# Kernel optimization log

Measured on AMD Instinct MI355X. Metric: run time of the kernel, lower is better.

## Reference

```python
import jax, jax.numpy as jnp
from jax import lax
import numpy as np

B, N, NF, EF, MD = 16, 128, 9, 3, 5
H, D, FF, L, O = 24, 768, 3072, 12, 128
NA, NID, NOD, NE, NS, NED = 4608, 256, 256, 1536, 512, 128
S = N + 1
EPS = 1e-5


def setup_inputs() -> dict:
    key = jax.random.key(0)
    ks = iter(jax.random.split(key, 64))
    emb_s = 0.02
    lin_s = 0.02 / np.sqrt(L)

    def nrm(shape, s):
        return jax.random.normal(next(ks), shape, jnp.float32) * s

    inp = {
        'x': jax.random.randint(next(ks), (B, N, NF), 0, NA + 1),
        'in_degree': jax.random.randint(next(ks), (B, N), 0, NID),
        'out_degree': jax.random.randint(next(ks), (B, N), 0, NOD),
        'spatial_pos': jax.random.randint(next(ks), (B, N, N), 0, NS),
        'edge_input': jax.random.randint(next(ks), (B, N, N, MD, EF), 0, NE + 1),
        'attn_bias': jnp.zeros((B, S, S), jnp.float32),
        # embeddings (padding_idx=0 rows zeroed)
        'atom_emb': nrm((NA + 1, D), emb_s).at[0].set(0.0),
        'in_deg_emb': nrm((NID, D), emb_s).at[0].set(0.0),
        'out_deg_emb': nrm((NOD, D), emb_s).at[0].set(0.0),
        'graph_token': nrm((1, D), emb_s),
        'edge_emb': nrm((NE + 1, H), emb_s).at[0].set(0.0),
        'edge_dis_emb': nrm((NED, H, H), emb_s),
        'spatial_emb': nrm((NS, H), emb_s).at[0].set(0.0),
        'virt_dist': nrm((1, H), emb_s),
        # stacked per-layer params
        'ln1_g': jnp.ones((L, D)), 'ln1_b': jnp.zeros((L, D)),
        'wq': nrm((L, D, D), lin_s), 'bq': jnp.zeros((L, D)),
        'wk': nrm((L, D, D), lin_s), 'bk': jnp.zeros((L, D)),
        'wv': nrm((L, D, D), lin_s), 'bv': jnp.zeros((L, D)),
        'wo': nrm((L, D, D), lin_s), 'bo': jnp.zeros((L, D)),
        'ln2_g': jnp.ones((L, D)), 'ln2_b': jnp.zeros((L, D)),
        'w1': nrm((L, D, FF), lin_s), 'b1': jnp.zeros((L, FF)),
        'w2': nrm((L, FF, D), lin_s), 'b2': jnp.zeros((L, D)),
        'final_g': jnp.ones((D,)), 'final_b': jnp.zeros((D,)),
        'out_w': nrm((D, O), lin_s), 'out_b': jnp.zeros((O,)),
    }
    return inp


def _ln(v, g, b):
    m = v.mean(-1, keepdims=True)
    va = ((v - m) ** 2).mean(-1, keepdims=True)
    return (v - m) / jnp.sqrt(va + EPS) * g + b


def _forward(x, in_degree, out_degree, spatial_pos, edge_input, attn_bias,
             atom_emb, in_deg_emb, out_deg_emb, graph_token,
             edge_emb, edge_dis_emb, spatial_emb, virt_dist,
             ln1_g, ln1_b, wq, bq, wk, bk, wv, bv, wo, bo,
             ln2_g, ln2_b, w1, b1, w2, b2, final_g, final_b, out_w, out_b):
    nb = x.shape[0]
    # ---- graph attn bias ----
    # spatial bias [B,H,N,N]
    sp_bias = spatial_emb[spatial_pos].transpose(0, 3, 1, 2)
    # multi-hop edge bias
    sp_ = jnp.where(spatial_pos == 0, 1, spatial_pos)
    sp_ = jnp.where(sp_ > 1, sp_ - 1, sp_)
    sp_ = jnp.clip(sp_, 0, MD)
    ei = edge_emb[edge_input].mean(-2)                       # [B,N,N,MD,H]
    eo = jnp.einsum('bijdh,dhk->bijk', ei, edge_dis_emb[:MD])
    edge_bias = (eo / sp_[..., None].astype(jnp.float32)).transpose(0, 3, 1, 2)
    t = virt_dist.reshape(1, H, 1)                           # virtual-token distance
    gab = jnp.repeat(attn_bias[:, None], H, axis=1)          # [B,H,S,S]
    gab = gab.at[:, :, 1:, 1:].add(sp_bias + edge_bias)
    gab = gab.at[:, :, 1:, 0].add(t)
    gab = gab.at[:, :, 0, :].add(t)
    gab = gab + attn_bias[:, None]
    # ---- node features ----
    nf = atom_emb[x].sum(-2) + in_deg_emb[in_degree] + out_deg_emb[out_degree]
    h = jnp.concatenate([jnp.broadcast_to(graph_token[None], (nb, 1, D)), nf], axis=1)  # [B,S,D]
    dk = D // H
    scale = dk ** -0.5

    def step(hc, p):
        (g1, b1n, Wq, Bq, Wk, Bk, Wv, Bv, Wo, Bo, g2, b2n, W1, B1, W2, B2) = p
        y = _ln(hc, g1, b1n)
        q = (y @ Wq + Bq).reshape(nb, S, H, dk).transpose(0, 2, 1, 3) * scale
        k = (y @ Wk + Bk).reshape(nb, S, H, dk).transpose(0, 2, 1, 3)
        v = (y @ Wv + Bv).reshape(nb, S, H, dk).transpose(0, 2, 1, 3)
        att = jnp.einsum('bhqd,bhkd->bhqk', q, k) + gab
        att = jax.nn.softmax(att, axis=-1)
        ctx = jnp.einsum('bhqk,bhkd->bhqd', att, v)
        ctx = ctx.transpose(0, 2, 1, 3).reshape(nb, S, D)
        hc = hc + (ctx @ Wo + Bo)
        y = _ln(hc, g2, b2n)
        y = jax.nn.gelu(y @ W1 + B1, approximate=False) @ W2 + B2
        return hc + y, None

    h, _ = lax.scan(step, h, (ln1_g, ln1_b, wq, bq, wk, bk, wv, bv, wo, bo,
                              ln2_g, ln2_b, w1, b1, w2, b2))
    h = _ln(h, final_g, final_b)
    return h[:, 0] @ out_w + out_b  # [B,O]


def reference(x, in_degree, out_degree, spatial_pos, edge_input, attn_bias,
              atom_emb, in_deg_emb, out_deg_emb, graph_token,
              edge_emb, edge_dis_emb, spatial_emb, virt_dist,
              ln1_g, ln1_b, wq, bq, wk, bk, wv, bv, wo, bo,
              ln2_g, ln2_b, w1, b1, w2, b2, final_g, final_b, out_w, out_b):
    return _forward(x, in_degree, out_degree, spatial_pos, edge_input, attn_bias,
                    atom_emb, in_deg_emb, out_deg_emb, graph_token,
                    edge_emb, edge_dis_emb, spatial_emb, virt_dist,
                    ln1_g, ln1_b, wq, bq, wk, bk, wv, bv, wo, bo,
                    ln2_g, ln2_b, w1, b1, w2, b2, final_g, final_b, out_w, out_b)
```

## Files before the change

kernel.cpp:

```cpp
#include <hip/hip_runtime.h>
#include <hip/hip_bf16.h>
#include <math.h>

typedef __hip_bfloat16 bf16;
typedef __attribute__((ext_vector_type(8))) short short8;
typedef __attribute__((ext_vector_type(4))) short short4v;
typedef __attribute__((ext_vector_type(4))) float f32x4;

constexpr int NB = 16;
constexpr int ND = 128;
constexpr int SQ = 129;
constexpr int NH = 24;
constexpr int DM = 768;
constexpr int DF = 3072;
constexpr int NLAY = 12;
constexpr int MROWS = NB * SQ;

__device__ __forceinline__ short f2bs(float f) {
  bf16 h = __float2bfloat16(f);
  return *(short*)&h;
}

__device__ __forceinline__ void gload16(const void* g, void* lds) {
  __builtin_amdgcn_global_load_lds(
      (const __attribute__((address_space(1))) unsigned int*)g,
      (__attribute__((address_space(3))) unsigned int*)lds, 16, 0, 0);
}

__global__ void k_nodefeat(const int* __restrict__ x, const int* __restrict__ ind,
                           const int* __restrict__ outd,
                           const float* __restrict__ atom, const float* __restrict__ ide,
                           const float* __restrict__ ode, const float* __restrict__ gtok,
                           float* __restrict__ h) {
  int bs = blockIdx.x;
  int b = bs / SQ, s = bs % SQ;
  int t = threadIdx.x;
  float* hrow = h + (size_t)bs * DM;
  if (s == 0) {
    for (int c = t; c < DM; c += 256) hrow[c] = gtok[c];
  } else {
    int n = s - 1;
    const int* xr = x + (b * ND + n) * 9;
    int a0 = xr[0], a1 = xr[1], a2 = xr[2], a3 = xr[3], a4 = xr[4];
    int a5 = xr[5], a6 = xr[6], a7 = xr[7], a8 = xr[8];
    int ii = ind[b * ND + n], oo = outd[b * ND + n];
    for (int c = t; c < DM; c += 256) {
      float acc = ide[(size_t)ii * DM + c] + ode[(size_t)oo * DM + c];
      acc += atom[(size_t)a0 * DM + c];
      acc += atom[(size_t)a1 * DM + c];
      acc += atom[(size_t)a2 * DM + c];
      acc += atom[(size_t)a3 * DM + c];
      acc += atom[(size_t)a4 * DM + c];
      acc += atom[(size_t)a5 * DM + c];
      acc += atom[(size_t)a6 * DM + c];
      acc += atom[(size_t)a7 * DM + c];
      acc += atom[(size_t)a8 * DM + c];
      hrow[c] = acc;
    }
  }
}

__global__ void k_gab_border(const float* __restrict__ ab, const float* __restrict__ virt,
                             float* __restrict__ gab) {
  int b = blockIdx.x;
  const int tot = NH * SQ + NH * ND;
  for (int idx = threadIdx.x; idx < tot; idx += 256) {
    if (idx < NH * SQ) {
      int hh = idx / SQ, j = idx % SQ;
      float v = 2.f * ab[((size_t)b * SQ + 0) * SQ + j] + virt[hh];
      gab[(((size_t)b * NH + hh) * SQ + 0) * SQ + j] = v;
    } else {
      int r = idx - NH * SQ;
      int hh = r / ND, i = r % ND + 1;
      float v = 2.f * ab[((size_t)b * SQ + i) * SQ + 0] + virt[hh];
      gab[(((size_t)b * NH + hh) * SQ + i) * SQ + 0] = v;
    }
  }
}

__global__ __launch_bounds__(256) void k_gab_edge(
    const int* __restrict__ spos, const int* __restrict__ eidx,
    const float* __restrict__ eemb, const float* __restrict__ edemb,
    const float* __restrict__ semb, const float* __restrict__ ab,
    float* __restrict__ gab) {
  __shared__ int eidxs[960];
  __shared__ short ei2[64 * 136];
  __shared__ short edT[32 * 136];
  __shared__ float ot[24][65];
  __shared__ float rinvA[64], a2A[64];
  __shared__ int spA[64];
  int bi = blockIdx.x;
  int half = bi & 1;
  int i = (bi >> 1) & 127;
  int b = bi >> 8;
  int j0 = half * 64;
  int t = threadIdx.x;
  const size_t rowbase = ((size_t)(b * ND + i)) * ND + j0;

  const int* esrc = eidx + rowbase * 15;
  for (int idx = t; idx < 960; idx += 256) eidxs[idx] = esrc[idx];
  for (int u = t; u < 720; u += 256) {
    int dh = u / 6, kq = u % 6;
    f32x4 v = *(const f32x4*)&edemb[dh * 24 + kq * 4];
    edT[(kq * 4 + 0) * 136 + dh] = f2bs(v[0]);
    edT[(kq * 4 + 1) * 136 + dh] = f2bs(v[1]);
    edT[(kq * 4 + 2) * 136 + dh] = f2bs(v[2]);
    edT[(kq * 4 + 3) * 136 + dh] = f2bs(v[3]);
  }
  for (int u = t; u < 1472; u += 256) {
    int k, dh;
    if (u < 384) { k = u >> 4; dh = 120 + (u & 15); }
    else { int v = u - 384; k = 24 + v / 136; dh = v % 136; }
    edT[k * 136 + dh] = 0;
  }
  if (t < 64) {
    int j = t;
    int sp = spos[rowbase + j];
    int spc = (sp == 0) ? 1 : sp;
    spc = (spc > 1) ? spc - 1 : spc;
    if (spc > 5) spc = 5;
    spA[j] = sp;
    rinvA[j] = 1.f / (float)spc;
    a2A[j] = 2.f * ab[((size_t)b * SQ + (i + 1)) * SQ + (j0 + j + 1)];
  }
  __syncthreads();

  {
    int j = t & 63, d = t >> 6;
#pragma unroll
    for (int pass = 0; pass < 2; pass++) {
      if (pass == 1) {
        if (t >= 64) break;
        j = t; d = 4;
      }
      const int* ep = &eidxs[j * 15 + d * 3];
      const float* r0 = eemb + (size_t)ep[0] * NH;
      const float* r1 = eemb + (size_t)ep[1] * NH;
      const float* r2 = eemb + (size_t)ep[2] * NH;
#pragma unroll
      for (int hq = 0; hq < 6; hq++) {
        f32x4 s = (*(const f32x4*)&r0[hq * 4] + *(const f32x4*)&r1[hq * 4] +
                   *(const f32x4*)&r2[hq * 4]) * (1.f / 3.f);
        short4v o;
        o[0] = f2bs(s[0]); o[1] = f2bs(s[1]); o[2] = f2bs(s[2]); o[3] = f2bs(s[3]);
        *(short4v*)&ei2[j * 136 + d * 24 + hq * 4] = o;
      }
    }
  }
  for (int idx = t; idx < 64 * 8; idx += 256) {
    int j = idx >> 3;
    ei2[j * 136 + 120 + (idx & 7)] = 0;
  }
  __syncthreads();

  int lane = t & 63, w = t >> 6;
  int fr = lane & 15, q = lane >> 4, fo = q * 8;
  f32x4 acc0 = {0.f, 0.f, 0.f, 0.f}, acc1 = {0.f, 0.f, 0.f, 0.f};
#pragma unroll
  for (int kk = 0; kk < 4; kk++) {
    short8 af = *(const short8*)&ei2[(w * 16 + fr) * 136 + kk * 32 + fo];
    short8 b0 = *(const short8*)&edT[(fr) * 136 + kk * 32 + fo];
    short8 b1 = *(const short8*)&edT[(16 + fr) * 136 + kk * 32 + fo];
    acc0 = __builtin_amdgcn_mfma_f32_16x16x32_bf16(af, b0, acc0, 0, 0, 0);
    acc1 = __builtin_amdgcn_mfma_f32_16x16x32_bf16(af, b1, acc1, 0, 0, 0);
  }
#pragma unroll
  for (int e = 0; e < 4; e++) {
    int j = w * 16 + q * 4 + e;
    ot[fr][j] = acc0[e];
    if (fr < 8) ot[16 + fr][j] = acc1[e];
  }
  __syncthreads();
  size_t obase = (((size_t)b * NH) * SQ + (i + 1)) * SQ + (j0 + 1);
  for (int idx = t; idx < 24 * 64; idx += 256) {
    int k = idx >> 6, j = idx & 63;
    float v = a2A[j] + semb[spA[j] * NH + k] + ot[k][j] * rinvA[j];
    gab[obase + (size_t)k * SQ * SQ + j] = v;
  }
}

struct Ptrs4 { const float* p[4]; };

template <int NW>
__global__ void k_transpose(Ptrs4 ps, short* __restrict__ dst, int R, int C,
                            size_t sstride) {
  __shared__ short tile[64][68];
  int z = blockIdx.z;
  const float* src = ps.p[z % NW] + (size_t)(z / NW) * sstride;
  short* d = dst + (size_t)z * (size_t)R * C;
  int r0 = blockIdx.x * 64, c0 = blockIdx.y * 64;
  int t = threadIdx.x;
  int tr = t >> 4, tc = (t & 15) * 4;
#pragma unroll
  for (int i = 0; i < 4; i++) {
    int r = tr + i * 16;
    f32x4 v = *(const f32x4*)(src + (size_t)(r0 + r) * C + c0 + tc);
    tile[r][tc + 0] = f2bs(v[0]);
    tile[r][tc + 1] = f2bs(v[1]);
    tile[r][tc + 2] = f2bs(v[2]);
    tile[r][tc + 3] = f2bs(v[3]);
  }
  __syncthreads();
#pragma unroll
  for (int i = 0; i < 4; i++) {
    int rr = tr + i * 16;
    short4v o;
    o[0] = tile[tc + 0][rr];
    o[1] = tile[tc + 1][rr];
    o[2] = tile[tc + 2][rr];
    o[3] = tile[tc + 3][rr];
    *(short4v*)(d + (size_t)(c0 + rr) * R + r0 + tc) = o;
  }
}

__global__ void k_ln(const float* __restrict__ h, const float* __restrict__ g,
                     const float* __restrict__ bb, bf16* __restrict__ y) {
  int r = blockIdx.x;
  int t = threadIdx.x, lane = t & 63, wid = t >> 6;
  __shared__ float red[8];
  const float* row = h + (size_t)r * DM;
  float v0 = row[t], v1 = row[t + 256], v2 = row[t + 512];
  float s = v0 + v1 + v2;
#pragma unroll
  for (int o = 32; o > 0; o >>= 1) s += __shfl_xor(s, o);
  if (lane == 0) red[wid] = s;
  __syncthreads();
  float mean = (red[0] + red[1] + red[2] + red[3]) * (1.f / 768.f);
  float d0 = v0 - mean, d1 = v1 - mean, d2 = v2 - mean;
  float q = d0 * d0 + d1 * d1 + d2 * d2;
#pragma unroll
  for (int o = 32; o > 0; o >>= 1) q += __shfl_xor(q, o);
  if (lane == 0) red[4 + wid] = q;
  __syncthreads();
  float var = (red[4] + red[5] + red[6] + red[7]) * (1.f / 768.f);
  float rstd = rsqrtf(var + 1e-5f);
  bf16* yr = y + (size_t)r * DM;
  yr[t] = __float2bfloat16(d0 * rstd * g[t] + bb[t]);
  yr[t + 256] = __float2bfloat16(d1 * rstd * g[t + 256] + bb[t + 256]);
  yr[t + 512] = __float2bfloat16(d2 * rstd * g[t + 512] + bb[t + 512]);
}

__global__ void k_ln_add2(float* __restrict__ h, const float* __restrict__ p0,
                          const float* __restrict__ p1, const float* __restrict__ cb,
                          const float* __restrict__ g, const float* __restrict__ bb,
                          bf16* __restrict__ y) {
  int r = blockIdx.x;
  int t = threadIdx.x, lane = t & 63, wid = t >> 6;
  __shared__ float red[8];
  size_t base = (size_t)r * DM;
  float v0 = h[base + t] + p0[base + t] + p1[base + t] + cb[t];
  float v1 = h[base + t + 256] + p0[base + t + 256] + p1[base + t + 256] + cb[t + 256];
  float v2 = h[base + t + 512] + p0[base + t + 512] + p1[base + t + 512] + cb[t + 512];
  h[base + t] = v0;
  h[base + t + 256] = v1;
  h[base + t + 512] = v2;
  float s = v0 + v1 + v2;
#pragma unroll
  for (int o = 32; o > 0; o >>= 1) s += __shfl_xor(s, o);
  if (lane == 0) red[wid] = s;
  __syncthreads();
  float mean = (red[0] + red[1] + red[2] + red[3]) * (1.f / 768.f);
  float d0 = v0 - mean, d1 = v1 - mean, d2 = v2 - mean;
  float q = d0 * d0 + d1 * d1 + d2 * d2;
#pragma unroll
  for (int o = 32; o > 0; o >>= 1) q += __shfl_xor(q, o);
  if (lane == 0) red[4 + wid] = q;
  __syncthreads();
  float var = (red[4] + red[5] + red[6] + red[7]) * (1.f / 768.f);
  float rstd = rsqrtf(var + 1e-5f);
  bf16* yr = y + base;
  yr[t] = __float2bfloat16(d0 * rstd * g[t] + bb[t]);
  yr[t + 256] = __float2bfloat16(d1 * rstd * g[t + 256] + bb[t + 256]);
  yr[t + 512] = __float2bfloat16(d2 * rstd * g[t + 512] + bb[t + 512]);
}

struct GemmPtrs {
  const short* bt[3];
  const float* bias[3];
  void* out[3];
  int aoff[3];
};

template <int MODE>
__device__ __forceinline__ void gemm_store(void* outp, size_t idx, float v) {
  if (MODE == 0 || MODE == 3) {
    ((float*)outp)[idx] = v;
  } else if (MODE == 4) {
    ((bf16*)outp)[idx] = __float2bfloat16(v);
  } else {
    float gg = 0.5f * v * (1.f + erff(v * 0.70710678118654752f));
    ((bf16*)outp)[idx] = __float2bfloat16(gg);
  }
}

template <int MODE>
__global__ __launch_bounds__(256, 3) void k_gemm128(const short* __restrict__ A, GemmPtrs p,
                                                    int M, int N, int K, int lda, int ldb) {
  __shared__ short At[128 * 64];
  __shared__ short Bt[128 * 64];
  int z = blockIdx.z;
  const short* BT = p.bt[z];
  const float* bias = p.bias[z];
  A += p.aoff[z];
  int m0 = blockIdx.x * 128, n0 = blockIdx.y * 128;
  int t = threadIdx.x, lane = t & 63, wid = t >> 6;
  int wr = wid >> 1, wc = wid & 1;
  f32x4 acc[4][4];
#pragma unroll
  for (int a = 0; a < 4; a++)
#pragma unroll
    for (int c = 0; c < 4; c++) acc[a][c] = (f32x4){0.f, 0.f, 0.f, 0.f};

  int lrow8 = lane >> 3;
  int lseg = (lane & 7) ^ lrow8;
  const short* gA[4];
  const short* gB[4];
#pragma unroll
  for (int i = 0; i < 4; i++) {
    int ar = m0 + wid * 32 + i * 8 + lrow8;
    if (ar >= M) ar = M - 1;
    gA[i] = A + (size_t)ar * lda + lseg * 8;
    int br = n0 + wid * 32 + i * 8 + lrow8;
    gB[i] = BT + (size_t)br * ldb + lseg * 8;
  }

  const int NIT = K >> 6;
  int fr = lane & 15, q = lane >> 4;
  for (int it = 0; it < NIT; ++it) {
    int k0 = it << 6;
#pragma unroll
    for (int i = 0; i < 4; i++) {
      gload16(gA[i] + k0, &At[(wid * 32 + i * 8) * 64]);
      gload16(gB[i] + k0, &Bt[(wid * 32 + i * 8) * 64]);
    }
    __syncthreads();
#pragma unroll
    for (int kk = 0; kk < 2; kk++) {
      int sg = ((q + kk * 4) ^ (fr & 7)) * 8;
      short8 af[4], bf[4];
#pragma unroll
      for (int mr = 0; mr < 4; mr++)
        af[mr] = *(const short8*)&At[(wr * 64 + mr * 16 + fr) * 64 + sg];
#pragma unroll
      for (int nc = 0; nc < 4; nc++)
        bf[nc] = *(const short8*)&Bt[(wc * 64 + nc * 16 + fr) * 64 + sg];
#pragma unroll
      for (int mr = 0; mr < 4; mr++)
#pragma unroll
        for (int nc = 0; nc < 4; nc++)
          acc[mr][nc] = __builtin_amdgcn_mfma_f32_16x16x32_bf16(af[mr], bf[nc], acc[mr][nc], 0, 0, 0);
    }
    __syncthreads();
  }

  int rsub = q * 4;
#pragma unroll
  for (int nc = 0; nc < 4; nc++) {
    int col = n0 + wc * 64 + nc * 16 + fr;
    float bv = (MODE == 3) ? 0.f : bias[col];
#pragma unroll
    for (int mr = 0; mr < 4; mr++) {
#pragma unroll
      for (int e = 0; e < 4; e++) {
        int r = m0 + wr * 64 + mr * 16 + rsub + e;
        if (r < M) gemm_store<MODE>(p.out[z], (size_t)r * N + col, acc[mr][nc][e] + bv);
      }
    }
  }
}

template <int MODE>
__global__ __launch_bounds__(256, 4) void k_gemm64(const short* __restrict__ A, GemmPtrs p,
                                                   int M, int N, int K, int lda, int ldb) {
  __shared__ short At[64 * 64];
  __shared__ short Bt[128 * 64];
  int z = blockIdx.z;
  const short* BT = p.bt[z];
  const float* bias = p.bias[z];
  A += p.aoff[z];
  int m0 = blockIdx.x * 64, n0 = blockIdx.y * 128;
  int t = threadIdx.x, lane = t & 63, wid = t >> 6;
  int wr = wid >> 1, wc = wid & 1;
  f32x4 acc[2][4];
#pragma unroll
  for (int a = 0; a < 2; a++)
#pragma unroll
    for (int c = 0; c < 4; c++) acc[a][c] = (f32x4){0.f, 0.f, 0.f, 0.f};

  int lrow8 = lane >> 3;
  int lseg = (lane & 7) ^ lrow8;
  const short* gA[2];
  const short* gB[4];
#pragma unroll
  for (int i = 0; i < 2; i++) {
    int ar = m0 + wid * 16 + i * 8 + lrow8;
    if (ar >= M) ar = M - 1;
    gA[i] = A + (size_t)ar * lda + lseg * 8;
  }
#pragma unroll
  for (int i = 0; i < 4; i++) {
    int br = n0 + wid * 32 + i * 8 + lrow8;
    gB[i] = BT + (size_t)br * ldb + lseg * 8;
  }

  const int NIT = K >> 6;
  int fr = lane & 15, q = lane >> 4;
  for (int it = 0; it < NIT; ++it) {
    int k0 = it << 6;
#pragma unroll
    for (int i = 0; i < 2; i++) gload16(gA[i] + k0, &At[(wid * 16 + i * 8) * 64]);
#pragma unroll
    for (int i = 0; i < 4; i++) gload16(gB[i] + k0, &Bt[(wid * 32 + i * 8) * 64]);
    __syncthreads();
#pragma unroll
    for (int kk = 0; kk < 2; kk++) {
      int sg = ((q + kk * 4) ^ (fr & 7)) * 8;
      short8 af[2], bf[4];
#pragma unroll
      for (int mr = 0; mr < 2; mr++)
        af[mr] = *(const short8*)&At[(wr * 32 + mr * 16 + fr) * 64 + sg];
#pragma unroll
      for (int nc = 0; nc < 4; nc++)
        bf[nc] = *(const short8*)&Bt[(wc * 64 + nc * 16 + fr) * 64 + sg];
#pragma unroll
      for (int mr = 0; mr < 2; mr++)
#pragma unroll
        for (int nc = 0; nc < 4; nc++)
          acc[mr][nc] = __builtin_amdgcn_mfma_f32_16x16x32_bf16(af[mr], bf[nc], acc[mr][nc], 0, 0, 0);
    }
    __syncthreads();
  }

  int rsub = q * 4;
#pragma unroll
  for (int nc = 0; nc < 4; nc++) {
    int col = n0 + wc * 64 + nc * 16 + fr;
    float bv = (MODE == 3) ? 0.f : bias[col];
#pragma unroll
    for (int mr = 0; mr < 2; mr++) {
#pragma unroll
      for (int e = 0; e < 4; e++) {
        int r = m0 + wr * 32 + mr * 16 + rsub + e;
        if (r < M) gemm_store<MODE>(p.out[z], (size_t)r * N + col, acc[mr][nc][e] + bv);
      }
    }
  }
}

__global__ __launch_bounds__(256) void k_attn(const bf16* __restrict__ Q,
                                              const bf16* __restrict__ Kb,
                                              const bf16* __restrict__ Vb,
                                              const float* __restrict__ gab,
                                              bf16* __restrict__ ctx) {
  __shared__ short Ql[144 * 40];
  __shared__ short Kl[144 * 40];
  __shared__ short Vt[32 * 168];
  __shared__ short Pc[144 * 40];
  int bh = blockIdx.x;
  int b = bh / NH, hh = bh % NH;
  int t = threadIdx.x;
  for (int idx = t; idx < 32 * 40; idx += 256) {
    int d = idx / 40, kk = 128 + (idx % 40);
    Vt[d * 168 + kk] = 0;
  }
  for (int idx = t; idx < 129 * 4; idx += 256) {
    int s = idx >> 2, seg = idx & 3;
    size_t src = ((size_t)(b * SQ + s)) * DM + hh * 32 + seg * 8;
    *(short8*)&Ql[s * 40 + seg * 8] = *(const short8*)((const short*)Q + src);
    *(short8*)&Kl[s * 40 + seg * 8] = *(const short8*)((const short*)Kb + src);
  }
  for (int idx = t; idx < 15 * 4; idx += 256) {
    int s = 129 + (idx >> 2), seg = idx & 3;
    short8 zz = {0, 0, 0, 0, 0, 0, 0, 0};
    *(short8*)&Ql[s * 40 + seg * 8] = zz;
    *(short8*)&Kl[s * 40 + seg * 8] = zz;
  }
  for (int idx = t; idx < 129 * 4; idx += 256) {
    int kk = idx >> 2, seg = idx & 3;
    size_t src = ((size_t)(b * SQ + kk)) * DM + hh * 32 + seg * 8;
    short8 v = *(const short8*)((const short*)Vb + src);
#pragma unroll
    for (int j = 0; j < 8; j++) Vt[(seg * 8 + j) * 168 + kk] = v[j];
  }
  __syncthreads();

  int lane = t & 63, w = t >> 6;
  int c16 = lane & 15, q4 = lane >> 4;
  const float scale = 0.17677669529663689f;
  const float* gabp = gab + (((size_t)(b * NH + hh)) * SQ) * SQ;

  for (int mt = w; mt < 9; mt += 4) {
    f32x4 sc[9];
    short8 aq = *(const short8*)&Ql[(mt * 16 + c16) * 40 + q4 * 8];
#pragma unroll
    for (int nt = 0; nt < 9; nt++) {
      short8 bk = *(const short8*)&Kl[(nt * 16 + c16) * 40 + q4 * 8];
      f32x4 zz = {0.f, 0.f, 0.f, 0.f};
      sc[nt] = __builtin_amdgcn_mfma_f32_16x16x32_bf16(aq, bk, zz, 0, 0, 0);
    }
#pragma unroll
    for (int e = 0; e < 4; e++) {
      int row = mt * 16 + q4 * 4 + e;
      int rr = row < 129 ? row : 128;
      const float* grow = gabp + (size_t)rr * SQ;
      float mloc = -1e30f;
#pragma unroll
      for (int nt = 0; nt < 9; nt++) {
        int col = nt * 16 + c16;
        float s = (col < 129) ? (sc[nt][e] * scale + grow[col]) : -1e30f;
        sc[nt][e] = s;
        mloc = fmaxf(mloc, s);
      }
#pragma unroll
      for (int o = 1; o < 16; o <<= 1) mloc = fmaxf(mloc, __shfl_xor(mloc, o));
      float sum = 0.f;
#pragma unroll
      for (int nt = 0; nt < 9; nt++) {
        float pp = __expf(sc[nt][e] - mloc);
        sc[nt][e] = pp;
        sum += pp;
      }
#pragma unroll
      for (int o = 1; o < 16; o <<= 1) sum += __shfl_xor(sum, o);
      float inv = 1.f / sum;
#pragma unroll
      for (int nt = 0; nt < 9; nt++) sc[nt][e] *= inv;
    }
    f32x4 oacc0 = {0.f, 0.f, 0.f, 0.f}, oacc1 = {0.f, 0.f, 0.f, 0.f};
#pragma unroll
    for (int c = 0; c < 5; c++) {
#pragma unroll
      for (int u = 0; u < 2; u++) {
        int nt = c * 2 + u;
        if (nt < 9) {
#pragma unroll
          for (int e = 0; e < 4; e++)
            Pc[(mt * 16 + q4 * 4 + e) * 40 + u * 16 + c16] = f2bs(sc[nt][e]);
        } else {
#pragma unroll
          for (int e = 0; e < 4; e++)
            Pc[(mt * 16 + q4 * 4 + e) * 40 + u * 16 + c16] = 0;
        }
      }
      asm volatile("s_waitcnt lgkmcnt(0)" ::: "memory");
      __builtin_amdgcn_sched_barrier(0);
      short8 ap = *(const short8*)&Pc[(mt * 16 + c16) * 40 + q4 * 8];
      short8 bv0 = *(const short8*)&Vt[(c16) * 168 + c * 32 + q4 * 8];
      short8 bv1 = *(const short8*)&Vt[(16 + c16) * 168 + c * 32 + q4 * 8];
      oacc0 = __builtin_amdgcn_mfma_f32_16x16x32_bf16(ap, bv0, oacc0, 0, 0, 0);
      oacc1 = __builtin_amdgcn_mfma_f32_16x16x32_bf16(ap, bv1, oacc1, 0, 0, 0);
    }
#pragma unroll
    for (int e = 0; e < 4; e++) {
      int row = mt * 16 + q4 * 4 + e;
      if (row < 129) {
        size_t obase = ((size_t)(b * SQ + row)) * DM + hh * 32;
        ctx[obase + c16] = __float2bfloat16(oacc0[e]);
        ctx[obase + 16 + c16] = __float2bfloat16(oacc1[e]);
      }
    }
  }
}

__global__ void k_final_add2(const float* __restrict__ h, const float* __restrict__ p0,
                             const float* __restrict__ p1, const float* __restrict__ cb,
                             const float* __restrict__ g, const float* __restrict__ bb,
                             const float* __restrict__ ow, const float* __restrict__ ob,
                             float* __restrict__ out) {
  int b = blockIdx.x;
  int t = threadIdx.x, lane = t & 63, wid = t >> 6;
  __shared__ float red[8];
  __shared__ float yn[768];
  size_t base = (size_t)(b * SQ) * DM;
  float v0 = h[base + t] + p0[base + t] + p1[base + t] + cb[t];
  float v1 = h[base + t + 256] + p0[base + t + 256] + p1[base + t + 256] + cb[t + 256];
  float v2 = h[base + t + 512] + p0[base + t + 512] + p1[base + t + 512] + cb[t + 512];
  float s = v0 + v1 + v2;
#pragma unroll
  for (int o = 32; o > 0; o >>= 1) s += __shfl_xor(s, o);
  if (lane == 0) red[wid] = s;
  __syncthreads();
  float mean = (red[0] + red[1] + red[2] + red[3]) * (1.f / 768.f);
  float d0 = v0 - mean, d1 = v1 - mean, d2 = v2 - mean;
  float q = d0 * d0 + d1 * d1 + d2 * d2;
#pragma unroll
  for (int o = 32; o > 0; o >>= 1) q += __shfl_xor(q, o);
  if (lane == 0) red[4 + wid] = q;
  __syncthreads();
  float var = (red[4] + red[5] + red[6] + red[7]) * (1.f / 768.f);
  float rstd = rsqrtf(var + 1e-5f);
  yn[t] = d0 * rstd * g[t] + bb[t];
  yn[t + 256] = d1 * rstd * g[t + 256] + bb[t + 256];
  yn[t + 512] = d2 * rstd * g[t + 512] + bb[t + 512];
  __syncthreads();
  if (t < 128) {
    float acc = ob[t];
    for (int d = 0; d < 768; d++) acc += yn[d] * ow[d * 128 + t];
    out[b * 128 + t] = acc;
  }
}

extern "C" void kernel_launch(void* const* d_in, const int* in_sizes, int n_in,
                              void* d_out, int out_size, void* d_ws, size_t ws_size,
                              hipStream_t stream) {
  (void)in_sizes; (void)n_in; (void)out_size;
  const int* x     = (const int*)d_in[0];
  const int* ind   = (const int*)d_in[1];
  const int* outd  = (const int*)d_in[2];
  const int* spos  = (const int*)d_in[3];
  const int* eidx  = (const int*)d_in[4];
  const float* ab   = (const float*)d_in[5];
  const float* atom = (const float*)d_in[6];
  const float* ide  = (const float*)d_in[7];
  const float* ode  = (const float*)d_in[8];
  const float* gtok = (const float*)d_in[9];
  const float* eemb = (const float*)d_in[10];
  const float* edemb= (const float*)d_in[11];
  const float* semb = (const float*)d_in[12];
  const float* virt = (const float*)d_in[13];
  const float* ln1g = (const float*)d_in[14];
  const float* ln1b = (const float*)d_in[15];
  const float* wq  = (const float*)d_in[16];
  const float* bq   = (const float*)d_in[17];
  const float* wk  = (const float*)d_in[18];
  const float* bk   = (const float*)d_in[19];
  const float* wv  = (const float*)d_in[20];
  const float* bv   = (const float*)d_in[21];
  const float* wo  = (const float*)d_in[22];
  const float* bo   = (const float*)d_in[23];
  const float* ln2g = (const float*)d_in[24];
  const float* ln2b = (const float*)d_in[25];
  const float* w1  = (const float*)d_in[26];
  const float* b1   = (const float*)d_in[27];
  const float* w2  = (const float*)d_in[28];
  const float* b2   = (const float*)d_in[29];
  const float* fg   = (const float*)d_in[30];
  const float* fb   = (const float*)d_in[31];
  const float* ow   = (const float*)d_in[32];
  const float* ob   = (const float*)d_in[33];
  float* out = (float*)d_out;

  const int DD2 = DM * DM;
  const size_t WQKVO = (size_t)DD2;
  const size_t WFF = (size_t)DM * DF;

  char* ws = (char*)d_ws;
  size_t off = 0;
  auto alloc = [&](size_t bytes) -> void* {
    void* p = ws + off;
    off += (bytes + 255) & ~(size_t)255;
    return p;
  };
  float* gab = (float*)alloc((size_t)NB * NH * SQ * SQ * 4);
  float* h   = (float*)alloc((size_t)MROWS * DM * 4);
  bf16* y    = (bf16*)alloc((size_t)MROWS * DM * 2);
  bf16* qb   = (bf16*)alloc((size_t)MROWS * DM * 2);
  bf16* kb2  = (bf16*)alloc((size_t)MROWS * DM * 2);
  bf16* vb2  = (bf16*)alloc((size_t)MROWS * DM * 2);
  bf16* ctx  = (bf16*)alloc((size_t)MROWS * DM * 2);
  bf16* t1   = (bf16*)alloc((size_t)MROWS * DF * 2);
  float* p0  = (float*)alloc((size_t)MROWS * DM * 4);
  float* p1  = (float*)alloc((size_t)MROWS * DM * 4);

  size_t need_hoist = off + ((size_t)NLAY * 4 * WQKVO + 2 * (size_t)NLAY * WFF) * 2 + (1 << 20);
  bool hoist = ws_size >= need_hoist;
  short* wT  = (short*)alloc((hoist ? (size_t)NLAY * 4 * WQKVO : 4 * WQKVO) * 2);
  short* w1T = (short*)alloc((hoist ? (size_t)NLAY * WFF : WFF) * 2);
  short* w2T = (short*)alloc((hoist ? (size_t)NLAY * WFF : WFF) * 2);

  dim3 blk(256);
  k_nodefeat<<<dim3(NB * SQ), blk, 0, stream>>>(x, ind, outd, atom, ide, ode, gtok, h);
  k_gab_border<<<dim3(NB), blk, 0, stream>>>(ab, virt, gab);
  k_gab_edge<<<dim3(NB * ND * 2), blk, 0, stream>>>(spos, eidx, eemb, edemb, semb, ab, gab);

  if (hoist) {
    Ptrs4 pq; pq.p[0] = wq; pq.p[1] = wk; pq.p[2] = wv; pq.p[3] = wo;
    k_transpose<4><<<dim3(12, 12, 48), blk, 0, stream>>>(pq, wT, DM, DM, WQKVO);
    Ptrs4 pa; pa.p[0] = w1; pa.p[1] = pa.p[2] = pa.p[3] = w1;
    k_transpose<1><<<dim3(12, 48, 12), blk, 0, stream>>>(pa, w1T, DM, DF, WFF);
    Ptrs4 pb; pb.p[0] = w2; pb.p[1] = pb.p[2] = pb.p[3] = w2;
    k_transpose<1><<<dim3(48, 12, 12), blk, 0, stream>>>(pb, w2T, DF, DM, WFF);
  }

  for (int l = 0; l < NLAY; l++) {
    if (!hoist) {
      Ptrs4 pq;
      pq.p[0] = wq + (size_t)l * DD2; pq.p[1] = wk + (size_t)l * DD2;
      pq.p[2] = wv + (size_t)l * DD2; pq.p[3] = wo + (size_t)l * DD2;
      k_transpose<4><<<dim3(12, 12, 4), blk, 0, stream>>>(pq, wT, DM, DM, 0);
      Ptrs4 pa; pa.p[0] = w1 + (size_t)l * WFF; pa.p[1] = pa.p[2] = pa.p[3] = pa.p[0];
      k_transpose<1><<<dim3(12, 48, 1), blk, 0, stream>>>(pa, w1T, DM, DF, 0);
      Ptrs4 pb; pb.p[0] = w2 + (size_t)l * WFF; pb.p[1] = pb.p[2] = pb.p[3] = pb.p[0];
      k_transpose<1><<<dim3(48, 12, 1), blk, 0, stream>>>(pb, w2T, DF, DM, 0);
    }
    const short* wTl  = wT  + (hoist ? (size_t)l * 4 * WQKVO : 0);
    const short* w1Tl = w1T + (hoist ? (size_t)l * WFF : 0);
    const short* w2Tl = w2T + (hoist ? (size_t)l * WFF : 0);

    if (l == 0)
      k_ln<<<dim3(MROWS), blk, 0, stream>>>(h, ln1g, ln1b, y);

    GemmPtrs gq;
    gq.bt[0] = wTl; gq.bt[1] = wTl + DD2; gq.bt[2] = wTl + 2 * DD2;
    gq.bias[0] = bq + l * DM; gq.bias[1] = bk + l * DM; gq.bias[2] = bv + l * DM;
    gq.out[0] = qb; gq.out[1] = kb2; gq.out[2] = vb2;
    gq.aoff[0] = gq.aoff[1] = gq.aoff[2] = 0;
    k_gemm128<4><<<dim3(17, 6, 3), blk, 0, stream>>>((const short*)y, gq, MROWS, DM, DM, DM, DM);

    k_attn<<<dim3(NB * NH), blk, 0, stream>>>(qb, kb2, vb2, gab, ctx);

    GemmPtrs go;
    go.bt[0] = wTl + 3 * DD2; go.bt[1] = wTl + 3 * DD2 + 384;
    go.bias[0] = go.bias[1] = nullptr;
    go.out[0] = p0; go.out[1] = p1;
    go.aoff[0] = 0; go.aoff[1] = 384;
    go.bt[2] = go.bt[0]; go.out[2] = p0; go.aoff[2] = 0; go.bias[2] = nullptr;
    k_gemm64<3><<<dim3(33, 6, 2), blk, 0, stream>>>((const short*)ctx, go, MROWS, DM, 384, DM, DM);

    k_ln_add2<<<dim3(MROWS), blk, 0, stream>>>(h, p0, p1, bo + l * DM,
                                               ln2g + l * DM, ln2b + l * DM, y);

    GemmPtrs g1;
    g1.bt[0] = g1.bt[1] = g1.bt[2] = w1Tl;
    g1.bias[0] = g1.bias[1] = g1.bias[2] = b1 + l * DF;
    g1.out[0] = g1.out[1] = g1.out[2] = t1;
    g1.aoff[0] = g1.aoff[1] = g1.aoff[2] = 0;
    k_gemm128<2><<<dim3(17, 24, 1), blk, 0, stream>>>((const short*)y, g1, MROWS, DF, DM, DM, DM);

    GemmPtrs g2;
    g2.bt[0] = w2Tl; g2.bt[1] = w2Tl + 1536;
    g2.bias[0] = g2.bias[1] = nullptr;
    g2.out[0] = p0; g2.out[1] = p1;
    g2.aoff[0] = 0; g2.aoff[1] = 1536;
    g2.bt[2] = g2.bt[0]; g2.out[2] = p0; g2.aoff[2] = 0; g2.bias[2] = nullptr;
    k_gemm64<3><<<dim3(33, 6, 2), blk, 0, stream>>>((const short*)t1, g2, MROWS, DM, 1536, DF, DF);

    if (l < NLAY - 1) {
      k_ln_add2<<<dim3(MROWS), blk, 0, stream>>>(h, p0, p1, b2 + l * DM,
                                                 ln1g + (l + 1) * DM, ln1b + (l + 1) * DM, y);
    } else {
      k_final_add2<<<dim3(NB), blk, 0, stream>>>(h, p0, p1, b2 + l * DM, fg, fb, ow, ob, out);
    }
  }
}
```

Before: 1.698 ms.

## Double-buffer GEMM LDS tiles with BK=32 and drop split-K partials

Both GEMM kernels now use two LDS buffers with a 32-wide K step and prefetch the next tile while computing the current one, which removes one barrier per iteration. The output-projection and FFN2 GEMMs no longer split K into two z-slices writing separate partial buffers. The residual+LN kernels now read a single partial, which cuts memory traffic and frees the p1 buffer. In exchange, those two GEMMs launch half as many blocks with twice the K loop, so occupancy and parallelism drop for the 768-wide outputs.

```diff
diff --git a/kernel.cpp b/kernel.cpp
--- a/kernel.cpp
+++ b/kernel.cpp
@@ -240,17 +240,17 @@
   yr[t + 512] = __float2bfloat16(d2 * rstd * g[t + 512] + bb[t + 512]);
 }
 
-__global__ void k_ln_add2(float* __restrict__ h, const float* __restrict__ p0,
-                          const float* __restrict__ p1, const float* __restrict__ cb,
+__global__ void k_ln_add1(float* __restrict__ h, const float* __restrict__ p0,
+                          const float* __restrict__ cb,
                           const float* __restrict__ g, const float* __restrict__ bb,
                           bf16* __restrict__ y) {
   int r = blockIdx.x;
   int t = threadIdx.x, lane = t & 63, wid = t >> 6;
   __shared__ float red[8];
   size_t base = (size_t)r * DM;
-  float v0 = h[base + t] + p0[base + t] + p1[base + t] + cb[t];
-  float v1 = h[base + t + 256] + p0[base + t + 256] + p1[base + t + 256] + cb[t + 256];
-  float v2 = h[base + t + 512] + p0[base + t + 512] + p1[base + t + 512] + cb[t + 512];
+  float v0 = h[base + t] + p0[base + t] + cb[t];
+  float v1 = h[base + t + 256] + p0[base + t + 256] + cb[t + 256];
+  float v2 = h[base + t + 512] + p0[base + t + 512] + cb[t + 512];
   h[base + t] = v0;
   h[base + t + 256] = v1;
   h[base + t + 512] = v2;
@@ -296,8 +296,8 @@
 template <int MODE>
 __global__ __launch_bounds__(256, 3) void k_gemm128(const short* __restrict__ A, GemmPtrs p,
                                                     int M, int N, int K, int lda, int ldb) {
-  __shared__ short At[128 * 64];
-  __shared__ short Bt[128 * 64];
+  __shared__ short At[2][128 * 32];
+  __shared__ short Bt[2][128 * 32];
   int z = blockIdx.z;
   const short* BT = p.bt[z];
   const float* bias = p.bias[z];
@@ -311,45 +311,54 @@
 #pragma unroll
     for (int c = 0; c < 4; c++) acc[a][c] = (f32x4){0.f, 0.f, 0.f, 0.f};
 
-  int lrow8 = lane >> 3;
-  int lseg = (lane & 7) ^ lrow8;
-  const short* gA[4];
-  const short* gB[4];
-#pragma unroll
-  for (int i = 0; i < 4; i++) {
-    int ar = m0 + wid * 32 + i * 8 + lrow8;
+  int lrow = lane >> 2;
+  int lseg = (lane & 3) ^ ((lane >> 3) & 3);
+  const short* gA[2];
+  const short* gB[2];
+#pragma unroll
+  for (int i = 0; i < 2; i++) {
+    int ar = m0 + wid * 32 + i * 16 + lrow;
     if (ar >= M) ar = M - 1;
     gA[i] = A + (size_t)ar * lda + lseg * 8;
-    int br = n0 + wid * 32 + i * 8 + lrow8;
+    int br = n0 + wid * 32 + i * 16 + lrow;
     gB[i] = BT + (size_t)br * ldb + lseg * 8;
   }
 
-  const int NIT = K >> 6;
+  const int NIT = K >> 5;
+#pragma unroll
+  for (int i = 0; i < 2; i++) {
+    gload16(gA[i], &At[0][(wid * 32 + i * 16) * 32]);
+    gload16(gB[i], &Bt[0][(wid * 32 + i * 16) * 32]);
+  }
+  __syncthreads();
+
   int fr = lane & 15, q = lane >> 4;
+  int sg = (q ^ ((fr >> 1) & 3)) * 8;
   for (int it = 0; it < NIT; ++it) {
-    int k0 = it << 6;
-#pragma unroll
-    for (int i = 0; i < 4; i++) {
-      gload16(gA[i] + k0, &At[(wid * 32 + i * 8) * 64]);
-      gload16(gB[i] + k0, &Bt[(wid * 32 + i * 8) * 64]);
-    }
-    __syncthreads();
-#pragma unroll
-    for (int kk = 0; kk < 2; kk++) {
-      int sg = ((q + kk * 4) ^ (fr & 7)) * 8;
-      short8 af[4], bf[4];
-#pragma unroll
-      for (int mr = 0; mr < 4; mr++)
-        af[mr] = *(const short8*)&At[(wr * 64 + mr * 16 + fr) * 64 + sg];
+    int cur = it & 1;
+    if (it + 1 < NIT) {
+      int nxt = cur ^ 1;
+      int k0 = (it + 1) << 5;
+#pragma unroll
+      for (int i = 0; i < 2; i++) {
+        gload16(gA[i] + k0, &At[nxt][(wid * 32 + i * 16) * 32]);
+        gload16(gB[i] + k0, &Bt[nxt][(wid * 32 + i * 16) * 32]);
+      }
+    }
+    const short* Ab = At[cur];
+    const short* Bb = Bt[cur];
+    short8 af[4], bf[4];
+#pragma unroll
+    for (int mr = 0; mr < 4; mr++)
+      af[mr] = *(const short8*)&Ab[(wr * 64 + mr * 16 + fr) * 32 + sg];
+#pragma unroll
+    for (int nc = 0; nc < 4; nc++)
+      bf[nc] = *(const short8*)&Bb[(wc * 64 + nc * 16 + fr) * 32 + sg];
+#pragma unroll
+    for (int mr = 0; mr < 4; mr++)
 #pragma unroll
       for (int nc = 0; nc < 4; nc++)
-        bf[nc] = *(const short8*)&Bt[(wc * 64 + nc * 16 + fr) * 64 + sg];
-#pragma unroll
-      for (int mr = 0; mr < 4; mr++)
-#pragma unroll
-        for (int nc = 0; nc < 4; nc++)
-          acc[mr][nc] = __builtin_amdgcn_mfma_f32_16x16x32_bf16(af[mr], bf[nc], acc[mr][nc], 0, 0, 0);
-    }
+        acc[mr][nc] = __builtin_amdgcn_mfma_f32_16x16x32_bf16(af[mr], bf[nc], acc[mr][nc], 0, 0, 0);
     __syncthreads();
   }
 
@@ -372,8 +381,8 @@
 template <int MODE>
 __global__ __launch_bounds__(256, 4) void k_gemm64(const short* __restrict__ A, GemmPtrs p,
                                                    int M, int N, int K, int lda, int ldb) {
-  __shared__ short At[64 * 64];
-  __shared__ short Bt[128 * 64];
+  __shared__ short At[2][64 * 32];
+  __shared__ short Bt[2][128 * 32];
   int z = blockIdx.z;
   const short* BT = p.bt[z];
   const float* bias = p.bias[z];
@@ -387,47 +396,51 @@
 #pragma unroll
     for (int c = 0; c < 4; c++) acc[a][c] = (f32x4){0.f, 0.f, 0.f, 0.f};
 
-  int lrow8 = lane >> 3;
-  int lseg = (lane & 7) ^ lrow8;
-  const short* gA[2];
-  const short* gB[4];
+  int lrow = lane >> 2;
+  int lseg = (lane & 3) ^ ((lane >> 3) & 3);
+  int ar = m0 + wid * 16 + lrow;
+  if (ar >= M) ar = M - 1;
+  const short* gA0 = A + (size_t)ar * lda + lseg * 8;
+  const short* gB[2];
 #pragma unroll
   for (int i = 0; i < 2; i++) {
-    int ar = m0 + wid * 16 + i * 8 + lrow8;
-    if (ar >= M) ar = M - 1;
-    gA[i] = A + (size_t)ar * lda + lseg * 8;
-  }
-#pragma unroll
-  for (int i = 0; i < 4; i++) {
-    int br = n0 + wid * 32 + i * 8 + lrow8;
+    int br = n0 + wid * 32 + i * 16 + lrow;
     gB[i] = BT + (size_t)br * ldb + lseg * 8;
   }
 
-  const int NIT = K >> 6;
+  const int NIT = K >> 5;
+  {
+    gload16(gA0, &At[0][(wid * 16) * 32]);
+#pragma unroll
+    for (int i = 0; i < 2; i++) gload16(gB[i], &Bt[0][(wid * 32 + i * 16) * 32]);
+  }
+  __syncthreads();
+
   int fr = lane & 15, q = lane >> 4;
+  int sg = (q ^ ((fr >> 1) & 3)) * 8;
   for (int it = 0; it < NIT; ++it) {
-    int k0 = it << 6;
-#pragma unroll
-    for (int i = 0; i < 2; i++) gload16(gA[i] + k0, &At[(wid * 16 + i * 8) * 64]);
-#pragma unroll
-    for (int i = 0; i < 4; i++) gload16(gB[i] + k0, &Bt[(wid * 32 + i * 8) * 64]);
-    __syncthreads();
-#pragma unroll
-    for (int kk = 0; kk < 2; kk++) {
-      int sg = ((q + kk * 4) ^ (fr & 7)) * 8;
-      short8 af[2], bf[4];
-#pragma unroll
-      for (int mr = 0; mr < 2; mr++)
-        af[mr] = *(const short8*)&At[(wr * 32 + mr * 16 + fr) * 64 + sg];
+    int cur = it & 1;
+    if (it + 1 < NIT) {
+      int nxt = cur ^ 1;
+      int k0 = (it + 1) << 5;
+      gload16(gA0 + k0, &At[nxt][(wid * 16) * 32]);
+#pragma unroll
+      for (int i = 0; i < 2; i++) gload16(gB[i] + k0, &Bt[nxt][(wid * 32 + i * 16) * 32]);
+    }
+    const short* Ab = At[cur];
+    const short* Bb = Bt[cur];
+    short8 af[2], bf[4];
+#pragma unroll
+    for (int mr = 0; mr < 2; mr++)
+      af[mr] = *(const short8*)&Ab[(wr * 32 + mr * 16 + fr) * 32 + sg];
+#pragma unroll
+    for (int nc = 0; nc < 4; nc++)
+      bf[nc] = *(const short8*)&Bb[(wc * 64 + nc * 16 + fr) * 32 + sg];
+#pragma unroll
+    for (int mr = 0; mr < 2; mr++)
 #pragma unroll
       for (int nc = 0; nc < 4; nc++)
-        bf[nc] = *(const short8*)&Bt[(wc * 64 + nc * 16 + fr) * 64 + sg];
-#pragma unroll
-      for (int mr = 0; mr < 2; mr++)
-#pragma unroll
-        for (int nc = 0; nc < 4; nc++)
-          acc[mr][nc] = __builtin_amdgcn_mfma_f32_16x16x32_bf16(af[mr], bf[nc], acc[mr][nc], 0, 0, 0);
-    }
+        acc[mr][nc] = __builtin_amdgcn_mfma_f32_16x16x32_bf16(af[mr], bf[nc], acc[mr][nc], 0, 0, 0);
     __syncthreads();
   }
 
@@ -562,8 +575,8 @@
   }
 }
 
-__global__ void k_final_add2(const float* __restrict__ h, const float* __restrict__ p0,
-                             const float* __restrict__ p1, const float* __restrict__ cb,
+__global__ void k_final_add1(const float* __restrict__ h, const float* __restrict__ p0,
+                             const float* __restrict__ cb,
                              const float* __restrict__ g, const float* __restrict__ bb,
                              const float* __restrict__ ow, const float* __restrict__ ob,
                              float* __restrict__ out) {
@@ -572,9 +585,9 @@
   __shared__ float red[8];
   __shared__ float yn[768];
   size_t base = (size_t)(b * SQ) * DM;
-  float v0 = h[base + t] + p0[base + t] + p1[base + t] + cb[t];
-  float v1 = h[base + t + 256] + p0[base + t + 256] + p1[base + t + 256] + cb[t + 256];
-  float v2 = h[base + t + 512] + p0[base + t + 512] + p1[base + t + 512] + cb[t + 512];
+  float v0 = h[base + t] + p0[base + t] + cb[t];
+  float v1 = h[base + t + 256] + p0[base + t + 256] + cb[t + 256];
+  float v2 = h[base + t + 512] + p0[base + t + 512] + cb[t + 512];
   float s = v0 + v1 + v2;
 #pragma unroll
   for (int o = 32; o > 0; o >>= 1) s += __shfl_xor(s, o);
@@ -660,7 +673,6 @@
   bf16* ctx  = (bf16*)alloc((size_t)MROWS * DM * 2);
   bf16* t1   = (bf16*)alloc((size_t)MROWS * DF * 2);
   float* p0  = (float*)alloc((size_t)MROWS * DM * 4);
-  float* p1  = (float*)alloc((size_t)MROWS * DM * 4);
 
   size_t need_hoist = off + ((size_t)NLAY * 4 * WQKVO + 2 * (size_t)NLAY * WFF) * 2 + (1 << 20);
   bool hoist = ws_size >= need_hoist;
@@ -710,14 +722,13 @@
     k_attn<<<dim3(NB * NH), blk, 0, stream>>>(qb, kb2, vb2, gab, ctx);
 
     GemmPtrs go;
-    go.bt[0] = wTl + 3 * DD2; go.bt[1] = wTl + 3 * DD2 + 384;
-    go.bias[0] = go.bias[1] = nullptr;
-    go.out[0] = p0; go.out[1] = p1;
-    go.aoff[0] = 0; go.aoff[1] = 384;
-    go.bt[2] = go.bt[0]; go.out[2] = p0; go.aoff[2] = 0; go.bias[2] = nullptr;
-    k_gemm64<3><<<dim3(33, 6, 2), blk, 0, stream>>>((const short*)ctx, go, MROWS, DM, 384, DM, DM);
-
-    k_ln_add2<<<dim3(MROWS), blk, 0, stream>>>(h, p0, p1, bo + l * DM,
+    go.bt[0] = go.bt[1] = go.bt[2] = wTl + 3 * DD2;
+    go.bias[0] = go.bias[1] = go.bias[2] = nullptr;
+    go.out[0] = go.out[1] = go.out[2] = p0;
+    go.aoff[0] = go.aoff[1] = go.aoff[2] = 0;
+    k_gemm64<3><<<dim3(33, 6, 1), blk, 0, stream>>>((const short*)ctx, go, MROWS, DM, DM, DM, DM);
+
+    k_ln_add1<<<dim3(MROWS), blk, 0, stream>>>(h, p0, bo + l * DM,
                                                ln2g + l * DM, ln2b + l * DM, y);
 
     GemmPtrs g1;
@@ -728,18 +739,17 @@
     k_gemm128<2><<<dim3(17, 24, 1), blk, 0, stream>>>((const short*)y, g1, MROWS, DF, DM, DM, DM);
 
     GemmPtrs g2;
-    g2.bt[0] = w2Tl; g2.bt[1] = w2Tl + 1536;
-    g2.bias[0] = g2.bias[1] = nullptr;
-    g2.out[0] = p0; g2.out[1] = p1;
-    g2.aoff[0] = 0; g2.aoff[1] = 1536;
-    g2.bt[2] = g2.bt[0]; g2.out[2] = p0; g2.aoff[2] = 0; g2.bias[2] = nullptr;
-    k_gemm64<3><<<dim3(33, 6, 2), blk, 0, stream>>>((const short*)t1, g2, MROWS, DM, 1536, DF, DF);
+    g2.bt[0] = g2.bt[1] = g2.bt[2] = w2Tl;
+    g2.bias[0] = g2.bias[1] = g2.bias[2] = nullptr;
+    g2.out[0] = g2.out[1] = g2.out[2] = p0;
+    g2.aoff[0] = g2.aoff[1] = g2.aoff[2] = 0;
+    k_gemm64<3><<<dim3(33, 6, 1), blk, 0, stream>>>((const short*)t1, g2, MROWS, DM, DF, DF, DF);
 
     if (l < NLAY - 1) {
-      k_ln_add2<<<dim3(MROWS), blk, 0, stream>>>(h, p0, p1, b2 + l * DM,
+      k_ln_add1<<<dim3(MROWS), blk, 0, stream>>>(h, p0, b2 + l * DM,
                                                  ln1g + (l + 1) * DM, ln1b + (l + 1) * DM, y);
     } else {
-      k_final_add2<<<dim3(NB), blk, 0, stream>>>(h, p0, p1, b2 + l * DM, fg, fb, ow, ob, out);
-    }
-  }
-}
+      k_final_add1<<<dim3(NB), blk, 0, stream>>>(h, p0, b2 + l * DM, fg, fb, ow, ob, out);
+    }
+  }
+}
```

After: 2.061 ms. 21.4% more time.

## Fuse per-head QKV projection into attention kernel

Applied to the files above, without the earlier changes.

Removes the separate QKV GEMM and computes each head's Q, K and V slice inside the attention block, staging y and weight tiles in LDS and accumulating with MFMA. The Q/K/V intermediate buffers and their global round trip go away. In exchange, each of the 384 blocks rereads its batch's full 129x768 activation slice (24 times redundantly across heads), and its K-loop is serial with two barriers per step. The LDS union now reuses the probability buffer for the staging tiles.

```diff
diff --git a/kernel.cpp b/kernel.cpp
--- a/kernel.cpp
+++ b/kernel.cpp
@@ -15,6 +15,7 @@
 constexpr int DF = 3072;
 constexpr int NLAY = 12;
 constexpr int MROWS = NB * SQ;
+constexpr int DD2C = DM * DM;
 
 __device__ __forceinline__ short f2bs(float f) {
   bf16 h = __float2bfloat16(f);
@@ -283,10 +284,8 @@
 
 template <int MODE>
 __device__ __forceinline__ void gemm_store(void* outp, size_t idx, float v) {
-  if (MODE == 0 || MODE == 3) {
+  if (MODE == 3) {
     ((float*)outp)[idx] = v;
-  } else if (MODE == 4) {
-    ((bf16*)outp)[idx] = __float2bfloat16(v);
   } else {
     float gg = 0.5f * v * (1.f + erff(v * 0.70710678118654752f));
     ((bf16*)outp)[idx] = __float2bfloat16(gg);
@@ -447,44 +446,97 @@
   }
 }
 
-__global__ __launch_bounds__(256) void k_attn(const bf16* __restrict__ Q,
-                                              const bf16* __restrict__ Kb,
-                                              const bf16* __restrict__ Vb,
-                                              const float* __restrict__ gab,
-                                              bf16* __restrict__ ctx) {
+__global__ __launch_bounds__(256) void k_fattn(const bf16* __restrict__ y,
+                                               const short* __restrict__ wTl,
+                                               const float* __restrict__ bq,
+                                               const float* __restrict__ bk,
+                                               const float* __restrict__ bv,
+                                               const float* __restrict__ gab,
+                                               bf16* __restrict__ ctx) {
   __shared__ short Ql[144 * 40];
   __shared__ short Kl[144 * 40];
   __shared__ short Vt[32 * 168];
-  __shared__ short Pc[144 * 40];
+  __shared__ short U[7680];
+  __shared__ float bqa[32], bka[32], bva[32];
+  short* Ay = U;
+  short* Bw = U + 144 * 32;
+  short* Pc = U;
   int bh = blockIdx.x;
   int b = bh / NH, hh = bh % NH;
   int t = threadIdx.x;
-  for (int idx = t; idx < 32 * 40; idx += 256) {
-    int d = idx / 40, kk = 128 + (idx % 40);
+  int lane = t & 63, w = t >> 6;
+
+  for (int idx = t; idx < 32 * 39; idx += 256) {
+    int d = idx / 39, kk = 129 + (idx % 39);
     Vt[d * 168 + kk] = 0;
   }
-  for (int idx = t; idx < 129 * 4; idx += 256) {
-    int s = idx >> 2, seg = idx & 3;
-    size_t src = ((size_t)(b * SQ + s)) * DM + hh * 32 + seg * 8;
-    *(short8*)&Ql[s * 40 + seg * 8] = *(const short8*)((const short*)Q + src);
-    *(short8*)&Kl[s * 40 + seg * 8] = *(const short8*)((const short*)Kb + src);
-  }
-  for (int idx = t; idx < 15 * 4; idx += 256) {
-    int s = 129 + (idx >> 2), seg = idx & 3;
-    short8 zz = {0, 0, 0, 0, 0, 0, 0, 0};
-    *(short8*)&Ql[s * 40 + seg * 8] = zz;
-    *(short8*)&Kl[s * 40 + seg * 8] = zz;
-  }
-  for (int idx = t; idx < 129 * 4; idx += 256) {
-    int kk = idx >> 2, seg = idx & 3;
-    size_t src = ((size_t)(b * SQ + kk)) * DM + hh * 32 + seg * 8;
-    short8 v = *(const short8*)((const short*)Vb + src);
-#pragma unroll
-    for (int j = 0; j < 8; j++) Vt[(seg * 8 + j) * 168 + kk] = v[j];
-  }
-  __syncthreads();
-
-  int lane = t & 63, w = t >> 6;
+  if (t < 32) {
+    bqa[t] = bq[hh * 32 + t];
+    bka[t] = bk[hh * 32 + t];
+    bva[t] = bv[hh * 32 + t];
+  }
+
+  f32x4 acc[3][3][2];
+#pragma unroll
+  for (int i = 0; i < 3; i++)
+#pragma unroll
+    for (int m = 0; m < 3; m++)
+#pragma unroll
+      for (int nt = 0; nt < 2; nt++) acc[i][m][nt] = (f32x4){0.f, 0.f, 0.f, 0.f};
+
+  int lr = lane >> 2;
+  int lsg = (lane & 3) ^ (lr & 3);
+  int fr = lane & 15, q = lane >> 4;
+  const short* ybase = (const short*)y + (size_t)(b * SQ) * DM;
+
+  for (int kt = 0; kt < 24; ++kt) {
+    __syncthreads();
+    for (int i = w; i < 9; i += 4) {
+      int grow_ = i * 16 + lr;
+      gload16(ybase + (size_t)grow_ * DM + kt * 32 + lsg * 8, &Ay[(i * 16) * 32]);
+    }
+    for (int i = w; i < 6; i += 4) {
+      int m = i >> 1, half = i & 1;
+      int nrow = hh * 32 + half * 16 + lr;
+      gload16(wTl + (size_t)m * DD2C + (size_t)nrow * DM + kt * 32 + lsg * 8,
+              &Bw[(m * 32 + half * 16) * 32]);
+    }
+    __syncthreads();
+    int sg = (q ^ (fr & 3)) * 8;
+#pragma unroll
+    for (int i = 0; i < 3; i++) {
+      int mt = w + 4 * i;
+      if (mt > 8) break;
+      short8 af = *(const short8*)&Ay[(mt * 16 + fr) * 32 + sg];
+#pragma unroll
+      for (int m = 0; m < 3; m++)
+#pragma unroll
+        for (int nt = 0; nt < 2; nt++) {
+          short8 bf = *(const short8*)&Bw[(m * 32 + nt * 16 + fr) * 32 + sg];
+          acc[i][m][nt] = __builtin_amdgcn_mfma_f32_16x16x32_bf16(af, bf, acc[i][m][nt], 0, 0, 0);
+        }
+    }
+  }
+  __syncthreads();
+#pragma unroll
+  for (int i = 0; i < 3; i++) {
+    int mt = w + 4 * i;
+    if (mt > 8) break;
+#pragma unroll
+    for (int nt = 0; nt < 2; nt++) {
+      int coll = nt * 16 + fr;
+      float bqv = bqa[coll], bkv = bka[coll], bvv = bva[coll];
+#pragma unroll
+      for (int e = 0; e < 4; e++) {
+        int row = mt * 16 + q * 4 + e;
+        Ql[row * 40 + coll] = f2bs(acc[i][0][nt][e] + bqv);
+        Kl[row * 40 + coll] = f2bs(acc[i][1][nt][e] + bkv);
+        if (row < 129) Vt[coll * 168 + row] = f2bs(acc[i][2][nt][e] + bvv);
+      }
+    }
+  }
+  __syncthreads();
+
   int c16 = lane & 15, q4 = lane >> 4;
   const float scale = 0.17677669529663689f;
   const float* gabp = gab + (((size_t)(b * NH + hh)) * SQ) * SQ;
@@ -494,9 +546,9 @@
     short8 aq = *(const short8*)&Ql[(mt * 16 + c16) * 40 + q4 * 8];
 #pragma unroll
     for (int nt = 0; nt < 9; nt++) {
-      short8 bk = *(const short8*)&Kl[(nt * 16 + c16) * 40 + q4 * 8];
+      short8 bk8 = *(const short8*)&Kl[(nt * 16 + c16) * 40 + q4 * 8];
       f32x4 zz = {0.f, 0.f, 0.f, 0.f};
-      sc[nt] = __builtin_amdgcn_mfma_f32_16x16x32_bf16(aq, bk, zz, 0, 0, 0);
+      sc[nt] = __builtin_amdgcn_mfma_f32_16x16x32_bf16(aq, bk8, zz, 0, 0, 0);
     }
 #pragma unroll
     for (int e = 0; e < 4; e++) {
@@ -654,9 +706,6 @@
   float* gab = (float*)alloc((size_t)NB * NH * SQ * SQ * 4);
   float* h   = (float*)alloc((size_t)MROWS * DM * 4);
   bf16* y    = (bf16*)alloc((size_t)MROWS * DM * 2);
-  bf16* qb   = (bf16*)alloc((size_t)MROWS * DM * 2);
-  bf16* kb2  = (bf16*)alloc((size_t)MROWS * DM * 2);
-  bf16* vb2  = (bf16*)alloc((size_t)MROWS * DM * 2);
   bf16* ctx  = (bf16*)alloc((size_t)MROWS * DM * 2);
   bf16* t1   = (bf16*)alloc((size_t)MROWS * DF * 2);
   float* p0  = (float*)alloc((size_t)MROWS * DM * 4);
@@ -700,14 +749,8 @@
     if (l == 0)
       k_ln<<<dim3(MROWS), blk, 0, stream>>>(h, ln1g, ln1b, y);
 
-    GemmPtrs gq;
-    gq.bt[0] = wTl; gq.bt[1] = wTl + DD2; gq.bt[2] = wTl + 2 * DD2;
-    gq.bias[0] = bq + l * DM; gq.bias[1] = bk + l * DM; gq.bias[2] = bv + l * DM;
-    gq.out[0] = qb; gq.out[1] = kb2; gq.out[2] = vb2;
-    gq.aoff[0] = gq.aoff[1] = gq.aoff[2] = 0;
-    k_gemm128<4><<<dim3(17, 6, 3), blk, 0, stream>>>((const short*)y, gq, MROWS, DM, DM, DM, DM);
-
-    k_attn<<<dim3(NB * NH), blk, 0, stream>>>(qb, kb2, vb2, gab, ctx);
+    k_fattn<<<dim3(NB * NH), blk, 0, stream>>>(y, wTl, bq + l * DM, bk + l * DM,
+                                               bv + l * DM, gab, ctx);
 
     GemmPtrs go;
     go.bt[0] = wTl + 3 * DD2; go.bt[1] = wTl + 3 * DD2 + 384;
```

After: 1.614 ms. -4.9%, faster.
